# Kernel tuning notes

Measured on AMD Instinct MI355X. Metric: run time of the kernel, lower is better.

## Reference

```python
import jax, jax.numpy as jnp
import numpy as np

B, S, E, H, D = 4, 2048, 1152, 12, 96
ROPE_BASE = 10000.0


def setup_inputs() -> dict:
    key = jax.random.key(0)
    ks = jax.random.split(key, 5)
    init = lambda k, shape: jax.random.normal(k, shape, dtype=jnp.float32) * 0.02
    return {
        "logits": jax.random.normal(ks[0], (B, S, E), dtype=jnp.float32),
        "Wq": init(ks[1], (E, H * D)), "bq": jnp.zeros((H * D,), jnp.float32),
        "Wk": init(ks[2], (E, H * D)), "bk": jnp.zeros((H * D,), jnp.float32),
        "Wv": init(ks[3], (E, H * D)), "bv": jnp.zeros((H * D,), jnp.float32),
        "Wo": init(ks[4], (H * D, E)), "bo": jnp.zeros((E,), jnp.float32),
        "batch_size": B,
        "seq_len": S,
    }


def _rope(x, cos, sin):
    # x: [b, s, h, d]; cos/sin: [s, d//2]; interleaved-pair rotation
    b, s, h, d = x.shape
    xr = x.reshape(b, s, h, d // 2, 2)
    c = cos[None, :, None, :]
    sn = sin[None, :, None, :]
    o0 = xr[..., 0] * c - xr[..., 1] * sn
    o1 = xr[..., 1] * c + xr[..., 0] * sn
    return jnp.stack([o0, o1], axis=-1).reshape(b, s, h, d)


def reference(logits, Wq, bq, Wk, bk, Wv, bv, Wo, bo, batch_size, seq_len):
    b, s = batch_size, seq_len
    q = (logits @ Wq + bq).reshape(b, s, H, D)
    k = (logits @ Wk + bk).reshape(b, s, H, D)
    v = (logits @ Wv + bv).reshape(b, s, H, D)

    # RoPE cache (cos/sin) for positions 0..s-1
    theta = 1.0 / (ROPE_BASE ** (jnp.arange(0, D, 2, dtype=jnp.float32) / D))  # [D/2]
    angles = jnp.arange(s, dtype=jnp.float32)[:, None] * theta[None, :]        # [s, D/2]
    cos, sin = jnp.cos(angles), jnp.sin(angles)

    q = _rope(q, cos, sin)
    k = _rope(k, cos, sin)

    # causal SDPA, scale = 1/sqrt(head_dim)
    scale = 1.0 / jnp.sqrt(jnp.asarray(D, jnp.float32))
    scores = jnp.einsum("bqhd,bkhd->bhqk", q, k) * scale  # [b, h, s, s]
    causal = jnp.tril(jnp.ones((s, s), dtype=bool))
    scores = jnp.where(causal[None, None], scores, -jnp.inf)
    attn = jax.nn.softmax(scores, axis=-1)
    ctx = jnp.einsum("bhqk,bkhd->bqhd", attn, v).reshape(b, s, H * D)
    return ctx @ Wo + bo
```

## Files before the change

### kernel.cpp

```cpp
#include <hip/hip_runtime.h>

typedef __bf16 bf16;
typedef bf16 bf16x4 __attribute__((ext_vector_type(4)));
typedef bf16 bf16x8 __attribute__((ext_vector_type(8)));
typedef float f32x4 __attribute__((ext_vector_type(4)));

#define B_  4
#define S_  2048
#define E_  1152
#define H_  12
#define D_  96
#define HD_ 1152
#define M_  (B_*S_)
#define BH_ (B_*H_)

__device__ __forceinline__ void gl2lds16(const void* g, void* l) {
    __builtin_amdgcn_global_load_lds((const __attribute__((address_space(1))) void*)g,
                                     (__attribute__((address_space(3))) void*)l, 16, 0, 0);
}

#define CAST_B_ 9216
#define TAB_B_  384
__global__ __launch_bounds__(256) void prep_k(const float* __restrict__ logits,
        bf16* __restrict__ Xbf, float2* __restrict__ ctab,
        const float* __restrict__ W0, const float* __restrict__ W1,
        const float* __restrict__ W2, const float* __restrict__ W3,
        bf16* __restrict__ T0, bf16* __restrict__ T1,
        bf16* __restrict__ T2, bf16* __restrict__ T3) {
    __shared__ float tsm[32][33];
    int bid = blockIdx.x, t = threadIdx.x;
    if (bid < CAST_B_) {
        size_t i = ((size_t)bid * 256 + t) * 4;
        float4 v = *(const float4*)(logits + i);
        bf16x4 o = { (bf16)v.x, (bf16)v.y, (bf16)v.z, (bf16)v.w };
        *(bf16x4*)(Xbf + i) = o;
    } else if (bid < CAST_B_ + TAB_B_) {
        int idx = (bid - CAST_B_) * 256 + t;
        int s = idx / 48, i = idx % 48;
        float theta = powf(10000.0f, -(float)(2 * i) / 96.0f);
        float ang = (float)s * theta;
        ctab[idx] = make_float2(cosf(ang), sinf(ang));
    } else {
        int tw = bid - (CAST_B_ + TAB_B_);
        int z = tw / 1296, rem = tw % 1296;
        const float* W; bf16* WT;
        switch (z) {
            case 0: W = W0; WT = T0; break;
            case 1: W = W1; WT = T1; break;
            case 2: W = W2; WT = T2; break;
            default: W = W3; WT = T3; break;
        }
        int bx = (rem % 36) * 32, by = (rem / 36) * 32;
        int tx = t & 31, ty = t >> 5;
        #pragma unroll
        for (int i = ty; i < 32; i += 8)
            tsm[i][tx] = W[(size_t)(by + i) * E_ + bx + tx];
        __syncthreads();
        #pragma unroll
        for (int i = ty; i < 32; i += 8)
            WT[(size_t)(bx + i) * E_ + by + tx] = (bf16)tsm[tx][i];
    }
}

__device__ __forceinline__ void gemm128_body(const bf16* __restrict__ X,
                                             const bf16* __restrict__ WT,
                                             const float* __restrict__ bias,
                                             bf16* __restrict__ Cb,
                                             float* __restrict__ Cf,
                                             const float2* __restrict__ ctab,
                                             int K, int mode, int m0, int n0) {
    __shared__ bf16 As[128 * 64];
    __shared__ bf16 Bs[128 * 64];
    const int N = 1152;
    int t = threadIdx.x;
    int lane = t & 63, wave = t >> 6;
    int quad = lane >> 4, l16 = lane & 15;
    int wm = wave >> 1, wn = wave & 1;

    int srow = t >> 3;
    int scol = ((t & 7) ^ (srow & 7)) * 8;
    const bf16* ga = X  + (size_t)(m0 + srow) * K + scol;
    const bf16* gb = WT + (size_t)(n0 + srow) * K + scol;
    bf16* la = As + t * 8;
    bf16* lb = Bs + t * 8;
    size_t skip = (size_t)32 * K;

    f32x4 acc[4][4];
    #pragma unroll
    for (int u = 0; u < 4; ++u)
        #pragma unroll
        for (int v = 0; v < 4; ++v) acc[u][v] = (f32x4){0.f, 0.f, 0.f, 0.f};

    for (int k0 = 0; k0 < K; k0 += 64) {
        __syncthreads();
        #pragma unroll
        for (int i = 0; i < 4; ++i) {
            gl2lds16(ga + k0 + i * skip, la + i * 2048);
            gl2lds16(gb + k0 + i * skip, lb + i * 2048);
        }
        __syncthreads();
        #pragma unroll
        for (int kk = 0; kk < 2; ++kk) {
            int xc = ((kk * 4 + quad) ^ (l16 & 7)) * 8;
            bf16x8 af[4], bfr[4];
            #pragma unroll
            for (int u = 0; u < 4; ++u)
                af[u] = *(const bf16x8*)(As + (wm * 64 + u * 16 + l16) * 64 + xc);
            #pragma unroll
            for (int v = 0; v < 4; ++v)
                bfr[v] = *(const bf16x8*)(Bs + (wn * 64 + v * 16 + l16) * 64 + xc);
            #pragma unroll
            for (int u = 0; u < 4; ++u)
                #pragma unroll
                for (int v = 0; v < 4; ++v)
                    acc[u][v] = __builtin_amdgcn_mfma_f32_16x16x32_bf16(af[u], bfr[v], acc[u][v], 0, 0, 0);
        }
    }

    int mrow = m0 + wm * 64, ncol = n0 + wn * 64;
    if (mode == 3) {
        #pragma unroll
        for (int v = 0; v < 4; ++v) {
            int n = ncol + v * 16 + l16;
            float bv = bias[n];
            #pragma unroll
            for (int u = 0; u < 4; ++u)
                #pragma unroll
                for (int r = 0; r < 4; ++r)
                    Cf[(size_t)(mrow + u * 16 + quad * 4 + r) * N + n] = acc[u][v][r] + bv;
        }
    } else if (mode == 1) {
        #pragma unroll
        for (int v = 0; v < 4; ++v) {
            int n = ncol + v * 16 + l16;
            float bv = bias[n];
            int i = (n % 96) >> 1;
            float sgn = (n & 1) ? 1.f : -1.f;
            #pragma unroll
            for (int u = 0; u < 4; ++u)
                #pragma unroll
                for (int r = 0; r < 4; ++r) {
                    int m = mrow + u * 16 + quad * 4 + r;
                    float x = acc[u][v][r] + bv;
                    float p = __shfl_xor(x, 1, 64);
                    float2 cs = ctab[(m & (S_ - 1)) * 48 + i];
                    Cb[(size_t)m * N + n] = (bf16)(x * cs.x + p * sgn * cs.y);
                }
        }
    } else if (mode == 2) {
        int bbase = (mrow >> 11) * H_;
        #pragma unroll
        for (int v = 0; v < 4; ++v) {
            int n = ncol + v * 16 + l16;
            int h = n / 96, d = n % 96;
            float bv = bias[n];
            bf16* vt = Cb + (size_t)((bbase + h) * 96 + d) * S_;
            #pragma unroll
            for (int u = 0; u < 4; ++u) {
                int s = (mrow + u * 16 + quad * 4) & (S_ - 1);
                bf16x4 val;
                #pragma unroll
                for (int r = 0; r < 4; ++r) val[r] = (bf16)(acc[u][v][r] + bv);
                *(bf16x4*)(vt + s) = val;
            }
        }
    } else {
        #pragma unroll
        for (int v = 0; v < 4; ++v) {
            int n = ncol + v * 16 + l16;
            float bv = bias[n];
            #pragma unroll
            for (int u = 0; u < 4; ++u)
                #pragma unroll
                for (int r = 0; r < 4; ++r)
                    Cb[(size_t)(mrow + u * 16 + quad * 4 + r) * N + n] = (bf16)(acc[u][v][r] + bv);
        }
    }
}

__global__ __launch_bounds__(256) void gemm_qkv_k(const bf16* __restrict__ X,
        const bf16* __restrict__ Wq, const bf16* __restrict__ Wk, const bf16* __restrict__ Wv,
        const float* __restrict__ bq, const float* __restrict__ bk, const float* __restrict__ bv,
        bf16* __restrict__ q, bf16* __restrict__ k, bf16* __restrict__ vt,
        const float2* __restrict__ ctab) {
    int zone = blockIdx.y / 9;
    int n0 = (blockIdx.y % 9) * 128;
    const bf16* W; const float* bias; bf16* C; int mode;
    if (zone == 0)      { W = Wq; bias = bq; C = q;  mode = 1; }
    else if (zone == 1) { W = Wk; bias = bk; C = k;  mode = 1; }
    else                { W = Wv; bias = bv; C = vt; mode = 2; }
    gemm128_body(X, W, bias, C, nullptr, ctab, E_, mode, blockIdx.x * 128, n0);
}

__global__ __launch_bounds__(256) void gemm_out_k(const bf16* __restrict__ X,
        const bf16* __restrict__ WT, const float* __restrict__ bias, float* __restrict__ Cf) {
    gemm128_body(X, WT, bias, nullptr, Cf, nullptr, HD_, 3, blockIdx.x * 128, blockIdx.y * 128);
}

__global__ __launch_bounds__(256) void flash4_k(const bf16* __restrict__ Q,
                                                const bf16* __restrict__ Kg,
                                                const bf16* __restrict__ VT,
                                                bf16* __restrict__ ctx) {
    __shared__ bf16 Ks[64 * 104];
    __shared__ bf16 Vs[96 * 72];
    __shared__ bf16 Ps[4][32][72];
    int t = threadIdx.x, lane = t & 63, wave = t >> 6;
    int quad = lane >> 4, l16 = lane & 15;
    int bh = blockIdx.x % BH_;
    int ch = (S_ / 128 - 1) - blockIdx.x / BH_;
    int b = bh / H_, h = bh % H_;
    int q0 = ch * 128;
    int qw = q0 + wave * 32;
    int qg0 = qw + l16, qg1 = qw + 16 + l16;

    const char* KbaseB = (const char*)(Kg + (size_t)(b * S_) * HD_ + h * D_);
    const char* VbaseB = (const char*)(VT + (size_t)(bh * D_) * S_);

    int krow[4], koff[4], vrow[4], voff[4];
    #pragma unroll
    for (int i = 0; i < 4; ++i) {
        int c = i * 256 + t;
        krow[i] = c / 13; koff[i] = (c % 13) * 16;
        vrow[i] = c / 9;  int cc = c % 9; voff[i] = ((cc == 8) ? 7 : cc) * 16;
    }

    const bf16* qrow0 = Q + (size_t)(b * S_ + qw + l16) * HD_ + h * D_;
    const bf16* qrow1 = qrow0 + (size_t)16 * HD_;
    bf16x8 qf0[3], qf1[3];
    #pragma unroll
    for (int c = 0; c < 3; ++c) {
        qf0[c] = *(const bf16x8*)(qrow0 + c * 32 + quad * 8);
        qf1[c] = *(const bf16x8*)(qrow1 + c * 32 + quad * 8);
    }

    f32x4 o0[6], o1[6];
    #pragma unroll
    for (int u = 0; u < 6; ++u) { o0[u] = (f32x4){0.f,0.f,0.f,0.f}; o1[u] = (f32x4){0.f,0.f,0.f,0.f}; }
    float ls0 = 0.f, ls1 = 0.f;
    const float K2 = 0.10206207261596575f * 1.4426950408889634f;
    int nk = q0 + 128;

    for (int kb = 0; kb < nk; kb += 64) {
        __syncthreads();
        const char* kg = KbaseB + (size_t)kb * (HD_ * 2);
        #pragma unroll
        for (int i = 0; i < 3; ++i)
            gl2lds16(kg + (size_t)krow[i] * (HD_ * 2) + koff[i], (char*)Ks + i * 4096 + t * 16);
        if (t < 64)
            gl2lds16(kg + (size_t)krow[3] * (HD_ * 2) + koff[3], (char*)Ks + 12288 + t * 16);
        #pragma unroll
        for (int i = 0; i < 4; ++i)
            if (i < 3 || t < 96)
                gl2lds16(VbaseB + (size_t)vrow[i] * (S_ * 2) + (size_t)kb * 2 + voff[i],
                         (char*)Vs + i * 4096 + t * 16);
        __syncthreads();

        f32x4 s0[4], s1[4];
        #pragma unroll
        for (int u = 0; u < 4; ++u) { s0[u] = (f32x4){0.f,0.f,0.f,0.f}; s1[u] = (f32x4){0.f,0.f,0.f,0.f}; }
        #pragma unroll
        for (int c = 0; c < 3; ++c)
            #pragma unroll
            for (int u = 0; u < 4; ++u) {
                bf16x8 kf = *(const bf16x8*)(Ks + (u * 16 + l16) * 104 + c * 32 + quad * 8);
                s0[u] = __builtin_amdgcn_mfma_f32_16x16x32_bf16(kf, qf0[c], s0[u], 0, 0, 0);
                s1[u] = __builtin_amdgcn_mfma_f32_16x16x32_bf16(kf, qf1[c], s1[u], 0, 0, 0);
            }

        #pragma unroll
        for (int u = 0; u < 4; ++u) {
            bf16x4 pv0, pv1;
            #pragma unroll
            for (int r = 0; r < 4; ++r) {
                int sidx = kb + u * 16 + quad * 4 + r;
                float e0 = __builtin_exp2f(s0[u][r] * K2);
                float e1 = __builtin_exp2f(s1[u][r] * K2);
                e0 = (sidx <= qg0) ? e0 : 0.f;
                e1 = (sidx <= qg1) ? e1 : 0.f;
                ls0 += e0; ls1 += e1;
                pv0[r] = (bf16)e0; pv1[r] = (bf16)e1;
            }
            *(bf16x4*)(&Ps[wave][l16][u * 16 + quad * 4])      = pv0;
            *(bf16x4*)(&Ps[wave][16 + l16][u * 16 + quad * 4]) = pv1;
        }
        asm volatile("s_waitcnt lgkmcnt(0)" ::: "memory");

        bf16x8 p00 = *(const bf16x8*)(&Ps[wave][l16][quad * 8]);
        bf16x8 p01 = *(const bf16x8*)(&Ps[wave][l16][32 + quad * 8]);
        bf16x8 p10 = *(const bf16x8*)(&Ps[wave][16 + l16][quad * 8]);
        bf16x8 p11 = *(const bf16x8*)(&Ps[wave][16 + l16][32 + quad * 8]);
        #pragma unroll
        for (int u = 0; u < 6; ++u) {
            bf16x8 v0 = *(const bf16x8*)(Vs + (u * 16 + l16) * 72 + quad * 8);
            o0[u] = __builtin_amdgcn_mfma_f32_16x16x32_bf16(v0, p00, o0[u], 0, 0, 0);
            o1[u] = __builtin_amdgcn_mfma_f32_16x16x32_bf16(v0, p10, o1[u], 0, 0, 0);
            bf16x8 v1 = *(const bf16x8*)(Vs + (u * 16 + l16) * 72 + 32 + quad * 8);
            o0[u] = __builtin_amdgcn_mfma_f32_16x16x32_bf16(v1, p01, o0[u], 0, 0, 0);
            o1[u] = __builtin_amdgcn_mfma_f32_16x16x32_bf16(v1, p11, o1[u], 0, 0, 0);
        }
    }

    ls0 += __shfl_xor(ls0, 16, 64); ls0 += __shfl_xor(ls0, 32, 64);
    ls1 += __shfl_xor(ls1, 16, 64); ls1 += __shfl_xor(ls1, 32, 64);
    float inv0 = 1.0f / ls0, inv1 = 1.0f / ls1;

    bf16* crow0 = ctx + (size_t)(b * S_ + qw + l16) * HD_ + h * D_;
    bf16* crow1 = crow0 + (size_t)16 * HD_;
    #pragma unroll
    for (int u = 0; u < 6; ++u) {
        bf16x4 a, c;
        #pragma unroll
        for (int r = 0; r < 4; ++r) { a[r] = (bf16)(o0[u][r] * inv0); c[r] = (bf16)(o1[u][r] * inv1); }
        *(bf16x4*)(crow0 + u * 16 + quad * 4) = a;
        *(bf16x4*)(crow1 + u * 16 + quad * 4) = c;
    }
}

extern "C" void kernel_launch(void* const* d_in, const int* in_sizes, int n_in,
                              void* d_out, int out_size, void* d_ws, size_t ws_size,
                              hipStream_t stream) {
    const float* logits = (const float*)d_in[0];
    const float* Wq = (const float*)d_in[1];
    const float* bq = (const float*)d_in[2];
    const float* Wk = (const float*)d_in[3];
    const float* bk = (const float*)d_in[4];
    const float* Wv = (const float*)d_in[5];
    const float* bv = (const float*)d_in[6];
    const float* Wo = (const float*)d_in[7];
    const float* bo = (const float*)d_in[8];
    float* out = (float*)d_out;

    char* ws = (char*)d_ws;
    size_t off = 0;
    auto alloc = [&](size_t bytes) { char* p = ws + off; off += (bytes + 255) & ~(size_t)255; return p; };
    bf16* Xbf = (bf16*)alloc((size_t)M_ * E_ * 2);
    bf16* WqT = (bf16*)alloc((size_t)E_ * HD_ * 2);
    bf16* WkT = (bf16*)alloc((size_t)E_ * HD_ * 2);
    bf16* WvT = (bf16*)alloc((size_t)E_ * HD_ * 2);
    bf16* WoT = (bf16*)alloc((size_t)HD_ * E_ * 2);
    bf16* qb  = (bf16*)alloc((size_t)M_ * HD_ * 2);
    bf16* kb  = (bf16*)alloc((size_t)M_ * HD_ * 2);
    bf16* VT  = (bf16*)alloc((size_t)M_ * HD_ * 2);
    float2* ctab = (float2*)alloc((size_t)S_ * 48 * 8);
    bf16* ctx = Xbf;

    hipLaunchKernelGGL(prep_k, dim3(CAST_B_ + TAB_B_ + 4 * 1296), dim3(256), 0, stream,
                       logits, Xbf, ctab, Wq, Wk, Wv, Wo, WqT, WkT, WvT, WoT);
    hipLaunchKernelGGL(gemm_qkv_k, dim3(M_ / 128, 27), dim3(256), 0, stream,
                       Xbf, WqT, WkT, WvT, bq, bk, bv, qb, kb, VT, ctab);
    hipLaunchKernelGGL(flash4_k, dim3(BH_ * (S_ / 128)), dim3(256), 0, stream, qb, kb, VT, ctx);
    hipLaunchKernelGGL(gemm_out_k, dim3(M_ / 128, 1152 / 128), dim3(256), 0, stream, ctx, WoT, bo, out);
}
```

Before: 329.6 us.

## Compute softmax row sums via MFMA ones-row and skip fully masked tiles

```diff
diff --git a/kernel.cpp b/kernel.cpp
--- a/kernel.cpp
+++ b/kernel.cpp
@@ -197,12 +197,12 @@
     gemm128_body(X, WT, bias, nullptr, Cf, nullptr, HD_, 3, blockIdx.x * 128, blockIdx.y * 128);
 }
 
-__global__ __launch_bounds__(256) void flash4_k(const bf16* __restrict__ Q,
+__global__ __launch_bounds__(256) void flash5_k(const bf16* __restrict__ Q,
                                                 const bf16* __restrict__ Kg,
                                                 const bf16* __restrict__ VT,
                                                 bf16* __restrict__ ctx) {
     __shared__ bf16 Ks[64 * 104];
-    __shared__ bf16 Vs[96 * 72];
+    __shared__ bf16 Vs[112 * 72];
     __shared__ bf16 Ps[4][32][72];
     int t = threadIdx.x, lane = t & 63, wave = t >> 6;
     int quad = lane >> 4, l16 = lane & 15;
@@ -213,6 +213,9 @@
     int qw = q0 + wave * 32;
     int qg0 = qw + l16, qg1 = qw + 16 + l16;
 
+    for (int j = t; j < 16 * 72; j += 256)
+        Vs[96 * 72 + j] = (j < 72) ? (bf16)1.0f : (bf16)0.0f;
+
     const char* KbaseB = (const char*)(Kg + (size_t)(b * S_) * HD_ + h * D_);
     const char* VbaseB = (const char*)(VT + (size_t)(bh * D_) * S_);
 
@@ -233,10 +236,9 @@
         qf1[c] = *(const bf16x8*)(qrow1 + c * 32 + quad * 8);
     }
 
-    f32x4 o0[6], o1[6];
-    #pragma unroll
-    for (int u = 0; u < 6; ++u) { o0[u] = (f32x4){0.f,0.f,0.f,0.f}; o1[u] = (f32x4){0.f,0.f,0.f,0.f}; }
-    float ls0 = 0.f, ls1 = 0.f;
+    f32x4 o0[7], o1[7];
+    #pragma unroll
+    for (int u = 0; u < 7; ++u) { o0[u] = (f32x4){0.f,0.f,0.f,0.f}; o1[u] = (f32x4){0.f,0.f,0.f,0.f}; }
     const float K2 = 0.10206207261596575f * 1.4426950408889634f;
     int nk = q0 + 128;
 
@@ -254,6 +256,8 @@
                 gl2lds16(VbaseB + (size_t)vrow[i] * (S_ * 2) + (size_t)kb * 2 + voff[i],
                          (char*)Vs + i * 4096 + t * 16);
         __syncthreads();
+
+        if (kb >= qw + 32) continue;
 
         f32x4 s0[4], s1[4];
         #pragma unroll
@@ -267,21 +271,33 @@
                 s1[u] = __builtin_amdgcn_mfma_f32_16x16x32_bf16(kf, qf1[c], s1[u], 0, 0, 0);
             }
 
-        #pragma unroll
-        for (int u = 0; u < 4; ++u) {
-            bf16x4 pv0, pv1;
-            #pragma unroll
-            for (int r = 0; r < 4; ++r) {
-                int sidx = kb + u * 16 + quad * 4 + r;
-                float e0 = __builtin_exp2f(s0[u][r] * K2);
-                float e1 = __builtin_exp2f(s1[u][r] * K2);
-                e0 = (sidx <= qg0) ? e0 : 0.f;
-                e1 = (sidx <= qg1) ? e1 : 0.f;
-                ls0 += e0; ls1 += e1;
-                pv0[r] = (bf16)e0; pv1[r] = (bf16)e1;
+        if (kb + 64 <= qw) {
+            #pragma unroll
+            for (int u = 0; u < 4; ++u) {
+                bf16x4 pv0, pv1;
+                #pragma unroll
+                for (int r = 0; r < 4; ++r) {
+                    pv0[r] = (bf16)__builtin_exp2f(s0[u][r] * K2);
+                    pv1[r] = (bf16)__builtin_exp2f(s1[u][r] * K2);
+                }
+                *(bf16x4*)(&Ps[wave][l16][u * 16 + quad * 4])      = pv0;
+                *(bf16x4*)(&Ps[wave][16 + l16][u * 16 + quad * 4]) = pv1;
             }
-            *(bf16x4*)(&Ps[wave][l16][u * 16 + quad * 4])      = pv0;
-            *(bf16x4*)(&Ps[wave][16 + l16][u * 16 + quad * 4]) = pv1;
+        } else {
+            #pragma unroll
+            for (int u = 0; u < 4; ++u) {
+                bf16x4 pv0, pv1;
+                #pragma unroll
+                for (int r = 0; r < 4; ++r) {
+                    int sidx = kb + u * 16 + quad * 4 + r;
+                    float e0 = __builtin_exp2f(s0[u][r] * K2);
+                    float e1 = __builtin_exp2f(s1[u][r] * K2);
+                    pv0[r] = (bf16)((sidx <= qg0) ? e0 : 0.f);
+                    pv1[r] = (bf16)((sidx <= qg1) ? e1 : 0.f);
+                }
+                *(bf16x4*)(&Ps[wave][l16][u * 16 + quad * 4])      = pv0;
+                *(bf16x4*)(&Ps[wave][16 + l16][u * 16 + quad * 4]) = pv1;
+            }
         }
         asm volatile("s_waitcnt lgkmcnt(0)" ::: "memory");
 
@@ -290,7 +306,7 @@
         bf16x8 p10 = *(const bf16x8*)(&Ps[wave][16 + l16][quad * 8]);
         bf16x8 p11 = *(const bf16x8*)(&Ps[wave][16 + l16][32 + quad * 8]);
         #pragma unroll
-        for (int u = 0; u < 6; ++u) {
+        for (int u = 0; u < 7; ++u) {
             bf16x8 v0 = *(const bf16x8*)(Vs + (u * 16 + l16) * 72 + quad * 8);
             o0[u] = __builtin_amdgcn_mfma_f32_16x16x32_bf16(v0, p00, o0[u], 0, 0, 0);
             o1[u] = __builtin_amdgcn_mfma_f32_16x16x32_bf16(v0, p10, o1[u], 0, 0, 0);
@@ -300,9 +316,8 @@
         }
     }
 
-    ls0 += __shfl_xor(ls0, 16, 64); ls0 += __shfl_xor(ls0, 32, 64);
-    ls1 += __shfl_xor(ls1, 16, 64); ls1 += __shfl_xor(ls1, 32, 64);
-    float inv0 = 1.0f / ls0, inv1 = 1.0f / ls1;
+    float inv0 = 1.0f / __shfl(o0[6][0], l16, 64);
+    float inv1 = 1.0f / __shfl(o1[6][0], l16, 64);
 
     bf16* crow0 = ctx + (size_t)(b * S_ + qw + l16) * HD_ + h * D_;
     bf16* crow1 = crow0 + (size_t)16 * HD_;
@@ -348,6 +363,6 @@
                        logits, Xbf, ctab, Wq, Wk, Wv, Wo, WqT, WkT, WvT, WoT);
     hipLaunchKernelGGL(gemm_qkv_k, dim3(M_ / 128, 27), dim3(256), 0, stream,
                        Xbf, WqT, WkT, WvT, bq, bk, bv, qb, kb, VT, ctab);
-    hipLaunchKernelGGL(flash4_k, dim3(BH_ * (S_ / 128)), dim3(256), 0, stream, qb, kb, VT, ctx);
+    hipLaunchKernelGGL(flash5_k, dim3(BH_ * (S_ / 128)), dim3(256), 0, stream, qb, kb, VT, ctx);
     hipLaunchKernelGGL(gemm_out_k, dim3(M_ / 128, 1152 / 128), dim3(256), 0, stream, ctx, WoT, bo, out);
 }
```

After: 318.6 us. -3.3%, faster.
